# Kernel tuning notes

Measured on AMD Instinct MI355X. Metric: run time of the kernel, lower is better.

## Reference

```python
import jax, jax.numpy as jnp
import numpy as np

N_NODES = 100000
N_EDGES = 1600000
D = 128
L = 3
BN_EPS = 1e-5


def setup_inputs() -> dict:
    key = jax.random.key(0)
    ks = jax.random.split(key, 6)
    x = jax.random.normal(ks[0], (N_NODES, D), dtype=jnp.float32)
    edge_index = jax.random.randint(ks[1], (2, N_EDGES), 0, N_NODES, dtype=jnp.int64)
    Wl = jax.random.normal(ks[2], (L, D, D), dtype=jnp.float32) / np.sqrt(D)
    bl = jax.random.normal(ks[3], (L, D), dtype=jnp.float32) * 0.01
    Wr = jax.random.normal(ks[4], (L, D, D), dtype=jnp.float32) / np.sqrt(D)
    gamma = jnp.ones((L, D), dtype=jnp.float32)
    beta = jnp.zeros((L, D), dtype=jnp.float32)
    return {"x": x, "edge_index": edge_index, "Wl": Wl, "bl": bl,
            "Wr": Wr, "gamma": gamma, "beta": beta}


def _sage_layer(x, src, dst, inv_deg, Wl_i, bl_i, Wr_i, gamma_i, beta_i):
    # mean aggregation over incoming edges: scatter-add messages then divide by degree
    agg_sum = jax.ops.segment_sum(x[src], dst, num_segments=N_NODES)  # [N, D]
    agg = agg_sum * inv_deg[:, None]
    # SAGEConv: lin_l(agg) (with bias) + lin_r(x) (no bias)
    h = jnp.einsum('nd,hd->nh', agg, Wl_i) + bl_i + jnp.einsum('nd,hd->nh', x, Wr_i)
    # BatchNorm1d (training-mode batch stats, biased variance)
    mean = jnp.mean(h, axis=0)
    var = jnp.mean(jnp.square(h - mean), axis=0)
    h = (h - mean) * jax.lax.rsqrt(var + BN_EPS) * gamma_i + beta_i
    return jax.nn.relu(h)  # dropout is identity in eval mode


def reference(x, edge_index, Wl, bl, Wr, gamma, beta):
    src, dst = edge_index[0], edge_index[1]
    deg = jax.ops.segment_sum(jnp.ones((N_EDGES,), jnp.float32), dst,
                              num_segments=N_NODES)
    inv_deg = 1.0 / jnp.maximum(deg, 1.0)
    for i in range(L):
        h = _sage_layer(x, src, dst, inv_deg, Wl[i], bl[i], Wr[i], gamma[i], beta[i])
        if 0 < i < L - 1:  # middle layers get a scaled residual (shapes match)
            x = x + 0.5 * h
        else:
            x = h
    return x
```

## Files before the change

kernel.cpp:

```cpp
#include <hip/hip_runtime.h>

#define N_NODES 100000
#define N_EDGES 1600000
#define D 128
#define BN_EPS 1e-5f
#define N_BLK ((N_NODES + 255) / 256)
#define N_GB ((N_NODES + 63) / 64)
#define NPART 8
#define FILL_BLOCKS 2048
#define NODES_PER_PART (N_NODES / NPART)

typedef short bf16x8 __attribute__((ext_vector_type(8)));
typedef float f32x4 __attribute__((ext_vector_type(4)));

__device__ inline unsigned short f32_to_bf16_rne(float f) {
    unsigned u = __builtin_bit_cast(unsigned, f);
    u += 0x7fffu + ((u >> 16) & 1u);
    return (unsigned short)(u >> 16);
}
__device__ inline float bf16lo_to_f32(unsigned v) { return __builtin_bit_cast(float, v << 16); }
__device__ inline float bf16hi_to_f32(unsigned v) { return __builtin_bit_cast(float, v & 0xffff0000u); }

__device__ inline void gload_lds16(const void* g, void* l) {
    __builtin_amdgcn_global_load_lds((const __attribute__((address_space(1))) unsigned*)g,
                                     (__attribute__((address_space(3))) unsigned*)l, 16, 0, 0);
}


__global__ __launch_bounds__(256) void k_deg(const int* __restrict__ dst, int* __restrict__ degi) {
    int e = blockIdx.x * 256 + threadIdx.x;
    if (e < N_EDGES) atomicAdd(&degi[dst[e]], 1);
}

__global__ __launch_bounds__(256) void k_blocksum(const int* __restrict__ degi, int* __restrict__ bsum) {
    __shared__ int sm[256];
    int t = threadIdx.x;
    int i = blockIdx.x * 256 + t;
    sm[t] = (i < N_NODES) ? degi[i] : 0;
    __syncthreads();
    for (int off = 128; off > 0; off >>= 1) {
        if (t < off) sm[t] += sm[t + off];
        __syncthreads();
    }
    if (t == 0) bsum[blockIdx.x] = sm[0];
}

__global__ __launch_bounds__(512) void k_scan_bsum(const int* __restrict__ bsum, int* __restrict__ boff) {
    __shared__ int sm[512];
    int t = threadIdx.x;
    int v = (t < N_BLK) ? bsum[t] : 0;
    sm[t] = v;
    __syncthreads();
    for (int off = 1; off < 512; off <<= 1) {
        int u = (t >= off) ? sm[t - off] : 0;
        __syncthreads();
        sm[t] += u;
        __syncthreads();
    }
    if (t < N_BLK) boff[t] = sm[t] - v;
}

__global__ __launch_bounds__(256) void k_rowptr(const int* __restrict__ degi, const int* __restrict__ boff,
                                                int* __restrict__ rowptr, float* __restrict__ inv_deg) {
    __shared__ int sm[256];
    int t = threadIdx.x;
    int i = blockIdx.x * 256 + t;
    int v = (i < N_NODES) ? degi[i] : 0;
    sm[t] = v;
    __syncthreads();
    for (int off = 1; off < 256; off <<= 1) {
        int u = (t >= off) ? sm[t - off] : 0;
        __syncthreads();
        sm[t] += u;
        __syncthreads();
    }
    if (i < N_NODES) {
        int incl = sm[t] + boff[blockIdx.x];
        rowptr[i] = incl - v;
        inv_deg[i] = 1.0f / fmaxf((float)v, 1.0f);
        if (i == N_NODES - 1) rowptr[N_NODES] = incl;
    }
}

__global__ __launch_bounds__(256) void k_fill(const int* __restrict__ src, const int* __restrict__ dst,
                                              const int* __restrict__ rowptr, int* __restrict__ cursor,
                                              int* __restrict__ colidx) {
    const int part = blockIdx.x & (NPART - 1);
    const int lo = part * NODES_PER_PART;
    const int hi = lo + NODES_PER_PART;
    const int stride = (FILL_BLOCKS / NPART) * 256;
    for (int e = (blockIdx.x >> 3) * 256 + threadIdx.x; e < N_EDGES; e += stride) {
        int d = dst[e];
        if (d >= lo && d < hi) {
            int pos = atomicAdd(&cursor[d], 1);
            colidx[rowptr[d] + pos] = src[e];
        }
    }
}


__global__ __launch_bounds__(256) void k_xconv(const float* __restrict__ src, unsigned short* __restrict__ hi) {
    int idx = blockIdx.x * 256 + threadIdx.x;
    if (idx >= N_NODES * 32) return;
    float4 v = ((const float4*)src)[idx];
    uint2 p;
    p.x = (unsigned)f32_to_bf16_rne(v.x) | ((unsigned)f32_to_bf16_rne(v.y) << 16);
    p.y = (unsigned)f32_to_bf16_rne(v.z) | ((unsigned)f32_to_bf16_rne(v.w) << 16);
    ((uint2*)hi)[idx] = p;
}

__global__ __launch_bounds__(256) void k_wconv(const float* __restrict__ src, unsigned short* __restrict__ hi,
                                               unsigned short* __restrict__ lo, int n) {
    int i = blockIdx.x * 256 + threadIdx.x;
    if (i >= n) return;
    float w = src[i];
    unsigned short h = f32_to_bf16_rne(w);
    float rem = w - bf16lo_to_f32((unsigned)h);
    hi[i] = h;
    lo[i] = f32_to_bf16_rne(rem);
}


__global__ __launch_bounds__(256) void k_agg(const unsigned short* __restrict__ xhi,
                                             const int* __restrict__ rowptr, const int* __restrict__ colidx,
                                             const float* __restrict__ inv_deg,
                                             unsigned short* __restrict__ agghi) {
    int wid = threadIdx.x >> 6;
    int l = threadIdx.x & 63;
    int n = blockIdx.x * 4 + wid;
    if (n >= N_NODES) return;
    int b = rowptr[n], e = rowptr[n + 1];
    const int half = l >> 5;
    const int cl = l & 31;
    float a0 = 0.f, a1 = 0.f, a2 = 0.f, a3 = 0.f;
    int i = b;
    for (; i + 8 <= e; i += 8) {
#pragma unroll
        for (int u = 0; u < 4; u++) {
            int s = colidx[i + u * 2 + half];
            uint2 v = *(const uint2*)(xhi + (size_t)s * D + cl * 4);
            a0 += bf16lo_to_f32(v.x); a1 += bf16hi_to_f32(v.x);
            a2 += bf16lo_to_f32(v.y); a3 += bf16hi_to_f32(v.y);
        }
    }
    for (; i + 2 <= e; i += 2) {
        int s = colidx[i + half];
        uint2 v = *(const uint2*)(xhi + (size_t)s * D + cl * 4);
        a0 += bf16lo_to_f32(v.x); a1 += bf16hi_to_f32(v.x);
        a2 += bf16lo_to_f32(v.y); a3 += bf16hi_to_f32(v.y);
    }
    if (i < e && half == 0) {
        int s = colidx[i];
        uint2 v = *(const uint2*)(xhi + (size_t)s * D + cl * 4);
        a0 += bf16lo_to_f32(v.x); a1 += bf16hi_to_f32(v.x);
        a2 += bf16lo_to_f32(v.y); a3 += bf16hi_to_f32(v.y);
    }
    a0 += __shfl_xor(a0, 32);
    a1 += __shfl_xor(a1, 32);
    a2 += __shfl_xor(a2, 32);
    a3 += __shfl_xor(a3, 32);
    if (half == 0) {
        float idg = inv_deg[n];
        uint2 p;
        p.x = (unsigned)f32_to_bf16_rne(a0 * idg) | ((unsigned)f32_to_bf16_rne(a1 * idg) << 16);
        p.y = (unsigned)f32_to_bf16_rne(a2 * idg) | ((unsigned)f32_to_bf16_rne(a3 * idg) << 16);
        *(uint2*)(agghi + (size_t)n * D + cl * 4) = p;
    }
}

__global__ __launch_bounds__(256, 2) void k_gemm(
    const unsigned short* __restrict__ agg_hi, const unsigned short* __restrict__ x_hi,
    const unsigned short* __restrict__ wl_hi, const unsigned short* __restrict__ wl_lo,
    const unsigned short* __restrict__ wr_hi, const unsigned short* __restrict__ wr_lo,
    const float* __restrict__ bl, unsigned short* __restrict__ h, float* __restrict__ partial) {
    __shared__ char lds[32768];
    const int t = threadIdx.x;
    const int w = t >> 6;
    const int l = t & 63;
    const int lr = l & 15;
    const int lg = l >> 4;
    const int base = blockIdx.x * 64;
    const int j0 = w * 32;

    {
#pragma unroll
        for (int i = 0; i < 8; i++) {
            int c = w * 8 + i;
            int ci = c & 15;
            int m = ci >> 2, kk = ci & 3;
            int n = base + m * 16 + lr;
            if (n > N_NODES - 1) n = N_NODES - 1;
            size_t goff = (size_t)n * 256 + kk * 64 + lg * 16;
            const char* srcp = ((c & 16) ? (const char*)x_hi : (const char*)agg_hi) + goff;
            gload_lds16(srcp, lds + c * 1024);
        }
    }

    f32x4 acc[4][2];
#pragma unroll
    for (int m = 0; m < 4; m++)
#pragma unroll
        for (int f = 0; f < 2; f++) acc[m][f] = (f32x4){0.f, 0.f, 0.f, 0.f};

#pragma unroll
    for (int seg = 0; seg < 2; seg++) {
        const unsigned short* WH = seg ? wr_hi : wl_hi;
        const unsigned short* WLo = seg ? wr_lo : wl_lo;
        bf16x8 wh[4][2], wlo[4][2];
#pragma unroll
        for (int kk = 0; kk < 4; kk++)
#pragma unroll
            for (int f = 0; f < 2; f++) {
                size_t wo = (size_t)(j0 + f * 16 + lr) * D + kk * 32 + lg * 8;
                wh[kk][f] = *(const bf16x8*)(WH + wo);
                wlo[kk][f] = *(const bf16x8*)(WLo + wo);
            }
        asm volatile("" :: "v"(wh[0][0]), "v"(wh[0][1]), "v"(wh[1][0]), "v"(wh[1][1]),
                           "v"(wh[2][0]), "v"(wh[2][1]), "v"(wh[3][0]), "v"(wh[3][1]));
        asm volatile("" :: "v"(wlo[0][0]), "v"(wlo[0][1]), "v"(wlo[1][0]), "v"(wlo[1][1]),
                           "v"(wlo[2][0]), "v"(wlo[2][1]), "v"(wlo[3][0]), "v"(wlo[3][1]));
        if (seg == 0) __syncthreads();
        const int tb = seg * 16384;
#pragma unroll
        for (int kk = 0; kk < 4; kk++) {
            bf16x8 a[4];
#pragma unroll
            for (int m = 0; m < 4; m++)
                a[m] = *(const bf16x8*)(lds + tb + (m * 4 + kk) * 1024 + l * 16);
#pragma unroll
            for (int f = 0; f < 2; f++)
#pragma unroll
                for (int m = 0; m < 4; m++) {
                    acc[m][f] = __builtin_amdgcn_mfma_f32_16x16x32_bf16(a[m], wh[kk][f], acc[m][f], 0, 0, 0);
                    acc[m][f] = __builtin_amdgcn_mfma_f32_16x16x32_bf16(a[m], wlo[kk][f], acc[m][f], 0, 0, 0);
                }
        }
    }

    float s1[2] = {0.f, 0.f}, s2[2] = {0.f, 0.f};
#pragma unroll
    for (int f = 0; f < 2; f++) {
        const int col = j0 + f * 16 + lr;
        const float bias = bl[col];
#pragma unroll
        for (int m = 0; m < 4; m++) {
#pragma unroll
            for (int r = 0; r < 4; r++) {
                int n = base + m * 16 + lg * 4 + r;
                if (n < N_NODES) {
                    float v = acc[m][f][r] + bias;
                    h[(size_t)n * D + col] = f32_to_bf16_rne(v);
                    s1[f] += v;
                    s2[f] += v * v;
                }
            }
        }
    }
#pragma unroll
    for (int f = 0; f < 2; f++) {
        s1[f] += __shfl_xor(s1[f], 16);
        s1[f] += __shfl_xor(s1[f], 32);
        s2[f] += __shfl_xor(s2[f], 16);
        s2[f] += __shfl_xor(s2[f], 32);
    }
    if (l < 16) {
        float* pp = partial + (size_t)blockIdx.x * 256;
        pp[j0 + l] = s1[0];
        pp[j0 + 16 + l] = s1[1];
        pp[128 + j0 + l] = s2[0];
        pp[128 + j0 + 16 + l] = s2[1];
    }
}

__global__ __launch_bounds__(256) void k_bnred(const float* __restrict__ partial, float* __restrict__ bnacc) {
    int t = threadIdx.x;
    float s = 0.f;
    for (int b = blockIdx.x; b < N_GB; b += gridDim.x)
        s += partial[(size_t)b * 256 + t];
    atomicAdd(&bnacc[t], s);
}

__global__ __launch_bounds__(256) void k_apply(const unsigned short* __restrict__ h,
                                               const float* __restrict__ bnacc,
                                               const float* __restrict__ gamma, const float* __restrict__ beta,
                                               const unsigned short* __restrict__ xres_hi,
                                               unsigned short* __restrict__ out_hi,
                                               float* __restrict__ out_f32, int mode) {
    __shared__ float sa[128], sc[128];
    int t = threadIdx.x;
    if (t < 128) {
        float mean = bnacc[t] * (1.0f / N_NODES);
        float var = bnacc[128 + t] * (1.0f / N_NODES) - mean * mean;
        float inv = rsqrtf(var + BN_EPS);
        float av = gamma[t] * inv;
        sa[t] = av;
        sc[t] = beta[t] - mean * av;
    }
    __syncthreads();
    int idx = blockIdx.x * 256 + t;
    if (idx >= N_NODES * 32) return;
    int c0 = (idx & 31) * 4;
    uint2 hv = ((const uint2*)h)[idx];
    float r0 = fmaxf(fmaf(bf16lo_to_f32(hv.x), sa[c0], sc[c0]), 0.f);
    float r1 = fmaxf(fmaf(bf16hi_to_f32(hv.x), sa[c0 + 1], sc[c0 + 1]), 0.f);
    float r2 = fmaxf(fmaf(bf16lo_to_f32(hv.y), sa[c0 + 2], sc[c0 + 2]), 0.f);
    float r3 = fmaxf(fmaf(bf16hi_to_f32(hv.y), sa[c0 + 3], sc[c0 + 3]), 0.f);
    if (mode == 1) {
        uint2 xv = ((const uint2*)xres_hi)[idx];
        r0 = fmaf(0.5f, r0, bf16lo_to_f32(xv.x));
        r1 = fmaf(0.5f, r1, bf16hi_to_f32(xv.x));
        r2 = fmaf(0.5f, r2, bf16lo_to_f32(xv.y));
        r3 = fmaf(0.5f, r3, bf16hi_to_f32(xv.y));
    }
    if (mode == 2) {
        ((float4*)out_f32)[idx] = make_float4(r0, r1, r2, r3);
    } else {
        uint2 p;
        p.x = (unsigned)f32_to_bf16_rne(r0) | ((unsigned)f32_to_bf16_rne(r1) << 16);
        p.y = (unsigned)f32_to_bf16_rne(r2) | ((unsigned)f32_to_bf16_rne(r3) << 16);
        ((uint2*)out_hi)[idx] = p;
    }
}


extern "C" void kernel_launch(void* const* d_in, const int* in_sizes, int n_in,
                              void* d_out, int out_size, void* d_ws, size_t ws_size,
                              hipStream_t stream) {
    const float* x_in = (const float*)d_in[0];
    const int* ei = (const int*)d_in[1];
    const float* Wl = (const float*)d_in[2];
    const float* bl = (const float*)d_in[3];
    const float* Wr = (const float*)d_in[4];
    const float* gamma = (const float*)d_in[5];
    const float* beta = (const float*)d_in[6];
    float* out = (float*)d_out;

    char* ws = (char*)d_ws;
    unsigned short* xhiA = (unsigned short*)ws; ws += (size_t)N_NODES * D * 2;
    unsigned short* xhiB = (unsigned short*)ws; ws += (size_t)N_NODES * D * 2;
    unsigned short* agghi = (unsigned short*)ws; ws += (size_t)N_NODES * D * 2;
    int* rowptr = (int*)ws; ws += (size_t)(N_NODES + 1) * 4;
    int* degi = (int*)ws; ws += (size_t)N_NODES * 4;
    int* cursor = (int*)ws; ws += (size_t)N_NODES * 4;
    int* colidx = (int*)ws; ws += (size_t)N_EDGES * 4;
    float* inv_deg = (float*)ws; ws += (size_t)N_NODES * 4;
    int* bsum = (int*)ws; ws += (size_t)N_BLK * 4;
    int* boff = (int*)ws; ws += (size_t)N_BLK * 4;
    unsigned short* wl_hi = (unsigned short*)ws; ws += (size_t)3 * D * D * 2;
    unsigned short* wl_lo = (unsigned short*)ws; ws += (size_t)3 * D * D * 2;
    unsigned short* wr_hi = (unsigned short*)ws; ws += (size_t)3 * D * D * 2;
    unsigned short* wr_lo = (unsigned short*)ws; ws += (size_t)3 * D * D * 2;
    float* partial = (float*)ws; ws += (size_t)N_GB * 256 * 4;
    float* bnacc = (float*)ws; ws += 256 * 4;

    const int* src = ei;
    const int* dst = ei + N_EDGES;

    hipMemsetAsync(degi, 0, (size_t)N_NODES * 4, stream);
    hipMemsetAsync(cursor, 0, (size_t)N_NODES * 4, stream);
    k_deg<<<(N_EDGES + 255) / 256, 256, 0, stream>>>(dst, degi);
    k_blocksum<<<N_BLK, 256, 0, stream>>>(degi, bsum);
    k_scan_bsum<<<1, 512, 0, stream>>>(bsum, boff);
    k_rowptr<<<N_BLK, 256, 0, stream>>>(degi, boff, rowptr, inv_deg);
    k_fill<<<FILL_BLOCKS, 256, 0, stream>>>(src, dst, rowptr, cursor, colidx);

    k_xconv<<<(N_NODES * 32 + 255) / 256, 256, 0, stream>>>(x_in, xhiA);
    k_wconv<<<(3 * D * D + 255) / 256, 256, 0, stream>>>(Wl, wl_hi, wl_lo, 3 * D * D);
    k_wconv<<<(3 * D * D + 255) / 256, 256, 0, stream>>>(Wr, wr_hi, wr_lo, 3 * D * D);

    unsigned short* xin[3] = { xhiA, xhiB, xhiA };
    unsigned short* xout[3] = { xhiB, xhiA, (unsigned short*)0 };
    int mode[3] = { 0, 1, 2 };

    for (int i = 0; i < 3; i++) {
        k_agg<<<(N_NODES + 3) / 4, 256, 0, stream>>>(xin[i], rowptr, colidx, inv_deg, agghi);
        k_gemm<<<N_GB, 256, 0, stream>>>(agghi, xin[i],
                                         wl_hi + (size_t)i * D * D, wl_lo + (size_t)i * D * D,
                                         wr_hi + (size_t)i * D * D, wr_lo + (size_t)i * D * D,
                                         bl + (size_t)i * D, agghi, partial);
        hipMemsetAsync(bnacc, 0, 256 * 4, stream);
        k_bnred<<<32, 256, 0, stream>>>(partial, bnacc);
        k_apply<<<(N_NODES * 32 + 255) / 256, 256, 0, stream>>>(agghi, bnacc,
                                                                gamma + (size_t)i * D, beta + (size_t)i * D,
                                                                xin[i], xout[i], out, mode[i]);
    }
}
```

Baseline: 612.6 us.

## Widen aggregation gathers to 16-byte loads with shuffled edge indices; drop BN atomics

```diff
diff --git a/kernel.cpp b/kernel.cpp
--- a/kernel.cpp
+++ b/kernel.cpp
@@ -125,46 +125,72 @@
                                              const int* __restrict__ rowptr, const int* __restrict__ colidx,
                                              const float* __restrict__ inv_deg,
                                              unsigned short* __restrict__ agghi) {
-    int wid = threadIdx.x >> 6;
-    int l = threadIdx.x & 63;
-    int n = blockIdx.x * 4 + wid;
+    const int wid = threadIdx.x >> 6;
+    const int l = threadIdx.x & 63;
+    const int n = blockIdx.x * 4 + wid;
     if (n >= N_NODES) return;
-    int b = rowptr[n], e = rowptr[n + 1];
-    const int half = l >> 5;
-    const int cl = l & 31;
-    float a0 = 0.f, a1 = 0.f, a2 = 0.f, a3 = 0.f;
+    const int b = rowptr[n], e = rowptr[n + 1];
+    const int c8 = l & 15;
+    const int g = l >> 4;
+    const size_t coff = (size_t)c8 * 16;
+
+    float acc[8];
+#pragma unroll
+    for (int k = 0; k < 8; k++) acc[k] = 0.f;
+
     int i = b;
-    for (; i + 8 <= e; i += 8) {
-#pragma unroll
-        for (int u = 0; u < 4; u++) {
-            int s = colidx[i + u * 2 + half];
-            uint2 v = *(const uint2*)(xhi + (size_t)s * D + cl * 4);
-            a0 += bf16lo_to_f32(v.x); a1 += bf16hi_to_f32(v.x);
-            a2 += bf16lo_to_f32(v.y); a3 += bf16hi_to_f32(v.y);
-        }
-    }
-    for (; i + 2 <= e; i += 2) {
-        int s = colidx[i + half];
-        uint2 v = *(const uint2*)(xhi + (size_t)s * D + cl * 4);
-        a0 += bf16lo_to_f32(v.x); a1 += bf16hi_to_f32(v.x);
-        a2 += bf16lo_to_f32(v.y); a3 += bf16hi_to_f32(v.y);
-    }
-    if (i < e && half == 0) {
-        int s = colidx[i];
-        uint2 v = *(const uint2*)(xhi + (size_t)s * D + cl * 4);
-        a0 += bf16lo_to_f32(v.x); a1 += bf16hi_to_f32(v.x);
-        a2 += bf16lo_to_f32(v.y); a3 += bf16hi_to_f32(v.y);
-    }
-    a0 += __shfl_xor(a0, 32);
-    a1 += __shfl_xor(a1, 32);
-    a2 += __shfl_xor(a2, 32);
-    a3 += __shfl_xor(a3, 32);
-    if (half == 0) {
+    while (i < e) {
+        int chunk = e - i; if (chunk > 64) chunk = 64;
+        int myE = colidx[i + (l < chunk ? l : chunk - 1)];
+        int j = 0;
+        for (; j + 8 <= chunk; j += 8) {
+            int s0 = __shfl(myE, j + g);
+            int s1 = __shfl(myE, j + 4 + g);
+            uint4 v0 = *(const uint4*)((const char*)xhi + (size_t)s0 * 256 + coff);
+            uint4 v1 = *(const uint4*)((const char*)xhi + (size_t)s1 * 256 + coff);
+            acc[0] += bf16lo_to_f32(v0.x); acc[1] += bf16hi_to_f32(v0.x);
+            acc[2] += bf16lo_to_f32(v0.y); acc[3] += bf16hi_to_f32(v0.y);
+            acc[4] += bf16lo_to_f32(v0.z); acc[5] += bf16hi_to_f32(v0.z);
+            acc[6] += bf16lo_to_f32(v0.w); acc[7] += bf16hi_to_f32(v0.w);
+            acc[0] += bf16lo_to_f32(v1.x); acc[1] += bf16hi_to_f32(v1.x);
+            acc[2] += bf16lo_to_f32(v1.y); acc[3] += bf16hi_to_f32(v1.y);
+            acc[4] += bf16lo_to_f32(v1.z); acc[5] += bf16hi_to_f32(v1.z);
+            acc[6] += bf16lo_to_f32(v1.w); acc[7] += bf16hi_to_f32(v1.w);
+        }
+        for (; j + 4 <= chunk; j += 4) {
+            int s0 = __shfl(myE, j + g);
+            uint4 v0 = *(const uint4*)((const char*)xhi + (size_t)s0 * 256 + coff);
+            acc[0] += bf16lo_to_f32(v0.x); acc[1] += bf16hi_to_f32(v0.x);
+            acc[2] += bf16lo_to_f32(v0.y); acc[3] += bf16hi_to_f32(v0.y);
+            acc[4] += bf16lo_to_f32(v0.z); acc[5] += bf16hi_to_f32(v0.z);
+            acc[6] += bf16lo_to_f32(v0.w); acc[7] += bf16hi_to_f32(v0.w);
+        }
+        if (j < chunk) {
+            int idx = j + g;
+            int s0 = __shfl(myE, idx < chunk ? idx : chunk - 1);
+            if (idx < chunk) {
+                uint4 v0 = *(const uint4*)((const char*)xhi + (size_t)s0 * 256 + coff);
+                acc[0] += bf16lo_to_f32(v0.x); acc[1] += bf16hi_to_f32(v0.x);
+                acc[2] += bf16lo_to_f32(v0.y); acc[3] += bf16hi_to_f32(v0.y);
+                acc[4] += bf16lo_to_f32(v0.z); acc[5] += bf16hi_to_f32(v0.z);
+                acc[6] += bf16lo_to_f32(v0.w); acc[7] += bf16hi_to_f32(v0.w);
+            }
+        }
+        i += chunk;
+    }
+#pragma unroll
+    for (int k = 0; k < 8; k++) {
+        acc[k] += __shfl_xor(acc[k], 16);
+        acc[k] += __shfl_xor(acc[k], 32);
+    }
+    if (g == 0) {
         float idg = inv_deg[n];
-        uint2 p;
-        p.x = (unsigned)f32_to_bf16_rne(a0 * idg) | ((unsigned)f32_to_bf16_rne(a1 * idg) << 16);
-        p.y = (unsigned)f32_to_bf16_rne(a2 * idg) | ((unsigned)f32_to_bf16_rne(a3 * idg) << 16);
-        *(uint2*)(agghi + (size_t)n * D + cl * 4) = p;
+        uint4 p;
+        p.x = (unsigned)f32_to_bf16_rne(acc[0] * idg) | ((unsigned)f32_to_bf16_rne(acc[1] * idg) << 16);
+        p.y = (unsigned)f32_to_bf16_rne(acc[2] * idg) | ((unsigned)f32_to_bf16_rne(acc[3] * idg) << 16);
+        p.z = (unsigned)f32_to_bf16_rne(acc[4] * idg) | ((unsigned)f32_to_bf16_rne(acc[5] * idg) << 16);
+        p.w = (unsigned)f32_to_bf16_rne(acc[6] * idg) | ((unsigned)f32_to_bf16_rne(acc[7] * idg) << 16);
+        *(uint4*)((char*)agghi + (size_t)n * 256 + coff) = p;
     }
 }
 
@@ -272,16 +298,16 @@
     }
 }
 
-__global__ __launch_bounds__(256) void k_bnred(const float* __restrict__ partial, float* __restrict__ bnacc) {
+__global__ __launch_bounds__(256) void k_bnred(const float* __restrict__ partial, float* __restrict__ bn32) {
     int t = threadIdx.x;
     float s = 0.f;
-    for (int b = blockIdx.x; b < N_GB; b += gridDim.x)
+    for (int b = blockIdx.x; b < N_GB; b += 32)
         s += partial[(size_t)b * 256 + t];
-    atomicAdd(&bnacc[t], s);
+    bn32[blockIdx.x * 256 + t] = s;
 }
 
 __global__ __launch_bounds__(256) void k_apply(const unsigned short* __restrict__ h,
-                                               const float* __restrict__ bnacc,
+                                               const float* __restrict__ bn32,
                                                const float* __restrict__ gamma, const float* __restrict__ beta,
                                                const unsigned short* __restrict__ xres_hi,
                                                unsigned short* __restrict__ out_hi,
@@ -289,8 +315,14 @@
     __shared__ float sa[128], sc[128];
     int t = threadIdx.x;
     if (t < 128) {
-        float mean = bnacc[t] * (1.0f / N_NODES);
-        float var = bnacc[128 + t] * (1.0f / N_NODES) - mean * mean;
+        float m1 = 0.f, m2 = 0.f;
+#pragma unroll 8
+        for (int i = 0; i < 32; i++) {
+            m1 += bn32[i * 256 + t];
+            m2 += bn32[i * 256 + 128 + t];
+        }
+        float mean = m1 * (1.0f / N_NODES);
+        float var = m2 * (1.0f / N_NODES) - mean * mean;
         float inv = rsqrtf(var + BN_EPS);
         float av = gamma[t] * inv;
         sa[t] = av;
@@ -351,7 +383,7 @@
     unsigned short* wr_hi = (unsigned short*)ws; ws += (size_t)3 * D * D * 2;
     unsigned short* wr_lo = (unsigned short*)ws; ws += (size_t)3 * D * D * 2;
     float* partial = (float*)ws; ws += (size_t)N_GB * 256 * 4;
-    float* bnacc = (float*)ws; ws += 256 * 4;
+    float* bn32 = (float*)ws; ws += 32 * 256 * 4;
 
     const int* src = ei;
     const int* dst = ei + N_EDGES;
@@ -378,9 +410,8 @@
                                          wl_hi + (size_t)i * D * D, wl_lo + (size_t)i * D * D,
                                          wr_hi + (size_t)i * D * D, wr_lo + (size_t)i * D * D,
                                          bl + (size_t)i * D, agghi, partial);
-        hipMemsetAsync(bnacc, 0, 256 * 4, stream);
-        k_bnred<<<32, 256, 0, stream>>>(partial, bnacc);
-        k_apply<<<(N_NODES * 32 + 255) / 256, 256, 0, stream>>>(agghi, bnacc,
+        k_bnred<<<32, 256, 0, stream>>>(partial, bn32);
+        k_apply<<<(N_NODES * 32 + 255) / 256, 256, 0, stream>>>(agghi, bn32,
                                                                 gamma + (size_t)i * D, beta + (size_t)i * D,
                                                                 xin[i], xout[i], out, mode[i]);
     }
```

Result: faster. 598.8 us (-2.2%).
